# Kernel tuning notes

Hardware: AMD Instinct MI355X
Metric: run time of the kernel (lower is better)

The kernel has to match this reference:

```python
import jax, jax.numpy as jnp
import numpy as np

N_AA = 21
A = 15
D_FEAT = 128
D_COORD = N_AA * A * 3            # 945
D_DIH = 3 * (3 * 2 * 2 + 1)       # 39
D_IN = D_FEAT + D_COORD + D_DIH + D_FEAT  # 1240
FREQ = np.array([1.0, 2.0, 3.0, 1.0, 0.5, 1.0 / 3.0], dtype=np.float32)


def setup_inputs() -> dict:
    key = jax.random.key(0)
    ks = jax.random.split(key, 16)
    B, L = 16, 2048
    seq_idx = jax.random.randint(ks[0], (B, L), 0, N_AA)
    xyz = jax.random.normal(ks[1], (B, L, A, 3), dtype=jnp.float32)
    orientation = jax.random.normal(ks[2], (B, L, 3, 3), dtype=jnp.float32)
    dihedrals = jax.random.normal(ks[3], (B, L, 3), dtype=jnp.float32)
    chain_idx = jax.random.randint(ks[4], (B, L), 0, 10)
    atom_mask = jnp.ones((B, L, A), dtype=jnp.float32)
    aa_emb = jax.random.normal(ks[5], (N_AA, D_FEAT), dtype=jnp.float32) * 0.02
    chain_emb = jax.random.normal(ks[6], (10, D_FEAT), dtype=jnp.float32) * 0.02
    chain_emb = chain_emb.at[0].set(0.0)  # padding_idx=0
    W1 = jax.random.normal(ks[7], (D_IN, 2 * D_FEAT), dtype=jnp.float32) * 0.02
    b1 = jnp.zeros((2 * D_FEAT,), dtype=jnp.float32)
    W2 = jax.random.normal(ks[8], (2 * D_FEAT, D_FEAT), dtype=jnp.float32) * 0.02
    b2 = jnp.zeros((D_FEAT,), dtype=jnp.float32)
    W3 = jax.random.normal(ks[9], (D_FEAT, D_FEAT), dtype=jnp.float32) * 0.02
    b3 = jnp.zeros((D_FEAT,), dtype=jnp.float32)
    W4 = jax.random.normal(ks[10], (D_FEAT, D_FEAT), dtype=jnp.float32) * 0.02
    b4 = jnp.zeros((D_FEAT,), dtype=jnp.float32)
    return {"seq_idx": seq_idx, "xyz": xyz, "orientation": orientation,
            "dihedrals": dihedrals, "chain_idx": chain_idx, "atom_mask": atom_mask,
            "aa_emb": aa_emb, "chain_emb": chain_emb,
            "W1": W1, "b1": b1, "W2": W2, "b2": b2,
            "W3": W3, "b3": b3, "W4": W4, "b4": b4}


def _forward(seq_idx, xyz, orientation, dihedrals, chain_idx, atom_mask,
             aa_emb, chain_emb, W1, b1, W2, b2, W3, b3, W4, b4):
    B, L = seq_idx.shape
    CA = 1
    aa_type_feat = aa_emb[seq_idx]                                  # [B,L,F]
    xyz_rel = xyz - xyz[:, :, CA:CA + 1, :]                         # [B,L,A,3]
    # xyz_local[...,a,i] = sum_j R[b,l,j,i] * xyz_rel[b,l,a,j] (R^T applied)
    xyz_local = jnp.einsum('blji,blaj->blai', orientation, xyz_rel)
    xyz_local = xyz_local * atom_mask[..., None]
    # one-hot scatter into the residue-type slot (equiv to expanded where-select)
    onehot = jax.nn.one_hot(seq_idx, N_AA, dtype=xyz.dtype)         # [B,L,T]
    coord_feat = jnp.einsum('blt,blad->bltad', onehot, xyz_local)
    coord_feat = coord_feat.reshape(B, L, D_COORD)
    # angular encoding of dihedrals
    x = dihedrals[..., None]                                        # [B,L,3,1]
    freq = jnp.asarray(FREQ, dtype=dihedrals.dtype)
    enc = jnp.concatenate([x, jnp.sin(freq * x), jnp.cos(freq * x)], axis=-1)
    dihedral_feat = enc.reshape(B, L, D_DIH)
    chain_feat = chain_emb[chain_idx]                               # [B,L,F]
    feats = jnp.concatenate([aa_type_feat, coord_feat, dihedral_feat, chain_feat], axis=-1)
    h = jax.nn.relu(feats @ W1 + b1)
    h = jax.nn.relu(h @ W2 + b2)
    h = jax.nn.relu(h @ W3 + b3)
    return h @ W4 + b4


def reference(seq_idx, xyz, orientation, dihedrals, chain_idx, atom_mask,
              aa_emb, chain_emb, W1, b1, W2, b2, W3, b3, W4, b4):
    return _forward(seq_idx, xyz, orientation, dihedrals, chain_idx, atom_mask,
                    aa_emb, chain_emb, W1, b1, W2, b2, W3, b3, W4, b4)
```

## Files before the change

### kernel.cpp

```cpp
#include <hip/hip_runtime.h>
#include <math.h>

#define N_AA 21
#define NATOM 15
#define DF 128
#define H1DIM 256
#define OFF_COORD 128
#define OFF_DIH 1073
#define OFF_CHAIN 1112
#define T 16
#define FT 32
#define DIH0 46
#define HS1 264
#define HS2 136
#define FS 104
#define NFRAG_CH 16
#define INVALID_IDX 0xFFFFFFFFu
#define SSTRIDE 260

#define PR_TAB 31
#define PR_WF 16
#define PR_WL 63

typedef __attribute__((ext_vector_type(8))) short s16x8;
typedef __attribute__((ext_vector_type(4))) float f32x4;

__constant__ float c_freq[6] = {1.0f, 2.0f, 3.0f, 1.0f, 0.5f, 1.0f / 3.0f};

#define FMA4(A, S, W)            \
  A.x = fmaf((S), (W).x, A.x);   \
  A.y = fmaf((S), (W).y, A.y);   \
  A.z = fmaf((S), (W).z, A.z);   \
  A.w = fmaf((S), (W).w, A.w);

__device__ inline float bf2f(unsigned short u) {
  union { unsigned int i; float f; } x;
  x.i = (unsigned)u << 16;
  return x.f;
}
__device__ inline unsigned short f2bf(float f) {
  unsigned int x = __float_as_uint(f);
  unsigned int r = (x + 0x7fffu + ((x >> 16) & 1u)) >> 16;
  return (unsigned short)r;
}

__global__ __launch_bounds__(256) void prep_all(
    const float* __restrict__ aa_emb, const float* __restrict__ chain_emb,
    const float* __restrict__ W1, const float* __restrict__ b1,
    const float* __restrict__ W2, const float* __restrict__ W3,
    const float* __restrict__ W4, const int* __restrict__ seq, int n,
    float* __restrict__ tabAA, float* __restrict__ tabCH,
    unsigned short* __restrict__ wf_hi, unsigned short* __restrict__ wf_lo,
    unsigned short* __restrict__ wl1, int* __restrict__ part) {
  __shared__ float s_stage[32 * SSTRIDE];
  __shared__ int s_h[N_AA];
  const int b = blockIdx.x;
  if (b < PR_TAB) {
    const int i = threadIdx.x;
    if (b < N_AA) {
      const float* e = aa_emb + b * DF;
      float acc = 0.f;
#pragma unroll 8
      for (int k = 0; k < DF; ++k) acc = fmaf(e[k], W1[k * H1DIM + i], acc);
      tabAA[b * H1DIM + i] = acc;
    } else {
      const int c = b - N_AA;
      const float* e = chain_emb + c * DF;
      float acc = b1[i];
#pragma unroll 8
      for (int k = 0; k < DF; ++k)
        acc = fmaf(e[k], W1[(OFF_CHAIN + k) * H1DIM + i], acc);
      tabCH[c * H1DIM + i] = acc;
    }
  } else if (b < PR_TAB + PR_WF) {
    const int cgb = b - PR_TAB;
    const float* W;
    int kbase;
    if (cgb < 8) { W = W2; kbase = cgb * 32; }
    else if (cgb < 12) { W = W3; kbase = (cgb - 8) * 32; }
    else { W = W4; kbase = (cgb - 12) * 32; }
    for (int idx = threadIdx.x; idx < 32 * 128; idx += 256) {
      const int k = idx >> 7, col = idx & 127;
      s_stage[k * SSTRIDE + col] = W[(kbase + k) * DF + col];
    }
    __syncthreads();
    for (int e = threadIdx.x; e < 8 * 512; e += 256) {
      const int rem = e & 511;
      const int nt = e >> 9;
      const int l = rem >> 3, jj = rem & 7;
      const int col = nt * 16 + (l & 15);
      const int k = (l >> 4) * 8 + jj;
      const float v = s_stage[k * SSTRIDE + col];
      const unsigned short h = f2bf(v);
      wf_hi[(size_t)cgb * 4096 + e] = h;
      wf_lo[(size_t)cgb * 4096 + e] = f2bf(v - bf2f(h));
    }
  } else if (b < PR_TAB + PR_WF + PR_WL) {
    const int b2 = b - PR_TAB - PR_WF;
    const int t = b2 / 3, c = b2 % 3;
    for (int idx = threadIdx.x; idx < 32 * 256; idx += 256) {
      const int kp = idx >> 8, col = idx & 255;
      const int k = c * 32 + kp;
      float v = 0.f;
      if (k < 45) v = W1[(OFF_COORD + t * 45 + k) * H1DIM + col];
      else if (k < 84) v = W1[(OFF_DIH + (k - 45)) * H1DIM + col];
      s_stage[kp * SSTRIDE + col] = v;
    }
    __syncthreads();
    for (int e = threadIdx.x; e < 16 * 512; e += 256) {
      const int rem = e & 511;
      const int nt = e >> 9;
      const int l = rem >> 3, j = rem & 7;
      const int col = nt * 16 + (l & 15);
      const int kp = (l >> 4) * 8 + j;
      wl1[(size_t)b2 * 8192 + e] = f2bf(s_stage[kp * SSTRIDE + col]);
    }
  } else {
    const int hb = b - PR_TAB - PR_WF - PR_WL;
    if (threadIdx.x < N_AA) s_h[threadIdx.x] = 0;
    __syncthreads();
    const int i = hb * 256 + threadIdx.x;
    if (i < n) atomicAdd(&s_h[seq[i]], 1);
    __syncthreads();
    if (threadIdx.x < N_AA) part[hb * N_AA + threadIdx.x] = s_h[threadIdx.x];
  }
}

__global__ __launch_bounds__(256) void scatter_pad(
    const int* __restrict__ seq, int n, int cap, int nblkH,
    const int* __restrict__ part, int* __restrict__ totals,
    unsigned int* __restrict__ perm) {
  __shared__ int ps_tot[N_AA][9];
  __shared__ int ps_base[N_AA][9];
  __shared__ int s_tot[N_AA];
  __shared__ int s_base[N_AA];
  __shared__ int s_off[N_AA + 1];
  __shared__ int h[N_AA];
  const int b = blockIdx.x;
  const int myhb = b - N_AA - 1;
  const int tid = threadIdx.x;
  const int segLen = (nblkH + 7) >> 3;
  if (tid < N_AA * 8) {
    const int t = tid >> 3, seg = tid & 7;
    int tot = 0, bas = 0;
    for (int j = 0; j < segLen; ++j) {
      const int hb = seg * segLen + j;
      if (hb < nblkH) {
        const int v = part[hb * N_AA + t];
        tot += v;
        if (hb < myhb) bas += v;
      }
    }
    ps_tot[t][seg] = tot;
    ps_base[t][seg] = bas;
  }
  __syncthreads();
  if (tid < N_AA) {
    int tot = 0, bas = 0;
#pragma unroll
    for (int s = 0; s < 8; ++s) { tot += ps_tot[tid][s]; bas += ps_base[tid][s]; }
    s_tot[tid] = tot;
    s_base[tid] = bas;
  }
  __syncthreads();
  if (tid == 0) {
    int acc = 0;
    s_off[0] = 0;
    for (int tt = 0; tt < N_AA; ++tt) {
      acc += (s_tot[tt] + 15) & ~15;
      s_off[tt + 1] = acc;
    }
  }
  __syncthreads();
  if (b < N_AA) {
    const int padstart = s_off[b] + s_tot[b];
    const int padcnt = s_off[b + 1] - padstart;
    if (tid < padcnt) perm[padstart + tid] = INVALID_IDX;
  } else if (b == N_AA) {
    for (int i = s_off[N_AA] + tid; i < cap; i += 256) perm[i] = INVALID_IDX;
    if (tid < N_AA) totals[tid] = s_tot[tid];
  } else {
    if (tid < N_AA) h[tid] = 0;
    __syncthreads();
    const int i = myhb * 256 + tid;
    if (i < n) {
      const int tt = seq[i];
      const int slot = atomicAdd(&h[tt], 1);
      perm[s_off[tt] + s_base[tt] + slot] = (unsigned int)i;
    }
  }
}

__global__ __launch_bounds__(256, 8) void residue_embed_sorted(
    const float* __restrict__ xyz, const float* __restrict__ orient,
    const float* __restrict__ dihedrals, const int* __restrict__ chain_idx,
    const float* __restrict__ amask, const float* __restrict__ b2,
    const float* __restrict__ b3, const float* __restrict__ b4,
    const float* __restrict__ tabAA, const float* __restrict__ tabCH,
    const unsigned short* __restrict__ wl1, const unsigned short* __restrict__ wf_hi,
    const unsigned short* __restrict__ wf_lo, const int* __restrict__ totals,
    const unsigned int* __restrict__ perm, float* __restrict__ out) {
  __shared__ unsigned short s_h1hi[T][HS1];
  __shared__ __align__(16) char s_u[T * HS2 * 2];
  __shared__ unsigned int s_g[T];
  __shared__ int s_c[T];
  __shared__ int s_off[N_AA + 1];
  __shared__ int s_cnt[N_AA];

  unsigned short (*s_fh)[FS] = (unsigned short(*)[FS])s_u;
  unsigned short (*s_h2hi)[HS2] = (unsigned short(*)[HS2])s_u;

  const int tid = threadIdx.x;
  const int base = blockIdx.x * T;

  if (tid < T) {
    const unsigned int g = perm[base + tid];
    s_g[tid] = g;
    s_c[tid] = (g != INVALID_IDX) ? chain_idx[g] : 0;
  }
  if (tid >= 32 && tid < 32 + N_AA) s_cnt[tid - 32] = totals[tid - 32];
  __syncthreads();
  if (tid == 0) {
    int acc = 0;
    s_off[0] = 0;
    for (int t2 = 0; t2 < N_AA; ++t2) {
      acc += (s_cnt[t2] + 15) & ~15;
      s_off[t2 + 1] = acc;
    }
  }

  for (int idx = tid; idx < T * 45; idx += 256) {
    const int r = idx / 45, k = idx % 45;
    const int a = k / 3, i = k % 3;
    const unsigned int g = s_g[r];
    float v = 0.f;
    if (g != INVALID_IDX) {
      const float* X = xyz + (size_t)g * 45;
      const float* R = orient + (size_t)g * 9;
      const float m = amask[(size_t)g * NATOM + a];
#pragma unroll
      for (int j = 0; j < 3; ++j)
        v = fmaf(R[j * 3 + i], X[a * 3 + j] - X[3 + j], v);
      v *= m;
    }
    s_fh[r][k] = f2bf(v);
  }
  for (int idx = tid; idx < T * 39; idx += 256) {
    const int r = idx / 39, kk = idx % 39;
    const int d = kk / 13, m = kk % 13;
    const unsigned int g = s_g[r];
    float v = 0.f;
    if (g != INVALID_IDX) {
      const float x = dihedrals[(size_t)g * 3 + d];
      if (m == 0) v = x;
      else if (m <= 6) v = sinf(c_freq[m - 1] * x);
      else v = cosf(c_freq[m - 7] * x);
    }
    s_fh[r][45 + kk] = f2bf(v);
  }
  for (int idx = tid; idx < T * 12; idx += 256) {
    const int r = idx / 12, k = 84 + idx % 12;
    s_fh[r][k] = 0;
  }
  __syncthreads();

  const int l = tid & 63;
  const int nc = tid >> 6;
  const int nc0 = nc * 32;
  const int ar = l & 15;
  const int kb = (l >> 4) * 8;
  const int drow = (l >> 4) * 4;
  const size_t fbase = (size_t)(2 * nc) * 512 + (size_t)l * 8;

  int ty = 0;
#pragma unroll
  for (int t2 = 1; t2 < N_AA; ++t2)
    if (base >= s_off[t2]) ty = t2;

  {
    f32x4 acc[4] = {{0.f, 0.f, 0.f, 0.f}, {0.f, 0.f, 0.f, 0.f},
                    {0.f, 0.f, 0.f, 0.f}, {0.f, 0.f, 0.f, 0.f}};
    s16x8 ah[3];
#pragma unroll
    for (int c = 0; c < 3; ++c)
      ah[c] = *(const s16x8*)(&s_fh[ar][c * 32 + kb]);
    const unsigned short* pB = wl1 + ((size_t)ty * 48 + 4 * nc) * 512 + (size_t)l * 8;
#pragma unroll
    for (int c = 0; c < 3; ++c) {
#pragma unroll
      for (int nt2 = 0; nt2 < 4; ++nt2) {
        const s16x8 bb = *(const s16x8*)(pB + ((size_t)c * 16 + nt2) * 512);
        acc[nt2] = __builtin_amdgcn_mfma_f32_16x16x32_bf16(ah[c], bb, acc[nt2], 0, 0, 0);
      }
    }
    __syncthreads();
#pragma unroll
    for (int nt2 = 0; nt2 < 4; ++nt2) {
      const int col0 = nc * 64 + nt2 * 16 + (l & 15);
      const float ta = tabAA[ty * H1DIM + col0];
#pragma unroll
      for (int reg = 0; reg < 4; ++reg) {
        const int row = drow + reg;
        float v = acc[nt2][reg] + ta + tabCH[s_c[row] * H1DIM + col0];
        v = fmaxf(v, 0.f);
        s_h1hi[row][col0] = f2bf(v);
      }
    }
  }
  __syncthreads();

#define MFMA_LAYER(NCHUNK, CG0, SRCH, SSTR, BPTR, EPI)                           \
  do {                                                                           \
    f32x4 acc0 = {0.f, 0.f, 0.f, 0.f}, acc1 = {0.f, 0.f, 0.f, 0.f};             \
    const unsigned short* ph = wf_hi + (size_t)(CG0)*4096 + fbase;               \
    const unsigned short* pl = wf_lo + (size_t)(CG0)*4096 + fbase;               \
    _Pragma("unroll 2")                                                          \
    for (int c = 0; c < (NCHUNK); ++c) {                                         \
      const s16x8 b0h = *(const s16x8*)(ph + (size_t)c * 4096);                  \
      const s16x8 b1h = *(const s16x8*)(ph + (size_t)c * 4096 + 512);            \
      const s16x8 b0l = *(const s16x8*)(pl + (size_t)c * 4096);                  \
      const s16x8 b1l = *(const s16x8*)(pl + (size_t)c * 4096 + 512);            \
      const int ko = c * 32 + kb;                                                \
      const s16x8 ah = *(const s16x8*)((SRCH) + ar * (SSTR) + ko);               \
      acc0 = __builtin_amdgcn_mfma_f32_16x16x32_bf16(ah, b0h, acc0, 0, 0, 0);    \
      acc1 = __builtin_amdgcn_mfma_f32_16x16x32_bf16(ah, b1h, acc1, 0, 0, 0);    \
      acc0 = __builtin_amdgcn_mfma_f32_16x16x32_bf16(ah, b0l, acc0, 0, 0, 0);    \
      acc1 = __builtin_amdgcn_mfma_f32_16x16x32_bf16(ah, b1l, acc1, 0, 0, 0);    \
    }                                                                            \
    const float bias0 = (BPTR)[nc0 + (l & 15)];                                  \
    const float bias1 = (BPTR)[nc0 + 16 + (l & 15)];                             \
    EPI                                                                          \
  } while (0)

#define EPI_HIDDEN(DH, DSTR)                                                     \
  {                                                                              \
    _Pragma("unroll")                                                            \
    for (int reg = 0; reg < 4; ++reg) {                                          \
      const int row = drow + reg;                                                \
      float v0 = fmaxf(acc0[reg] + bias0, 0.f);                                  \
      float v1 = fmaxf(acc1[reg] + bias1, 0.f);                                  \
      (DH)[row * (DSTR) + nc0 + (l & 15)] = f2bf(v0);                            \
      (DH)[row * (DSTR) + nc0 + 16 + (l & 15)] = f2bf(v1);                       \
    }                                                                            \
  }

  MFMA_LAYER(8, 0, &s_h1hi[0][0], HS1, b2, EPI_HIDDEN(&s_h2hi[0][0], HS2));
  __syncthreads();

  MFMA_LAYER(4, 8, &s_h2hi[0][0], HS2, b3, EPI_HIDDEN(&s_h1hi[0][0], HS1));
  __syncthreads();

  MFMA_LAYER(4, 12, &s_h1hi[0][0], HS1, b4, {
    _Pragma("unroll")
    for (int reg = 0; reg < 4; ++reg) {
      const unsigned int g = s_g[drow + reg];
      if (g != INVALID_IDX) {
        out[(size_t)g * DF + nc0 + (l & 15)] = acc0[reg] + bias0;
        out[(size_t)g * DF + nc0 + 16 + (l & 15)] = acc1[reg] + bias1;
      }
    }
  });
}

__global__ __launch_bounds__(256) void precompute_tables(
    const float* __restrict__ aa_emb, const float* __restrict__ chain_emb,
    const float* __restrict__ W1, const float* __restrict__ b1,
    float* __restrict__ tabAA, float* __restrict__ tabCH) {
  const int i = threadIdx.x;
  const int b = blockIdx.x;
  if (b < N_AA) {
    const float* e = aa_emb + b * DF;
    float acc = 0.f;
#pragma unroll 8
    for (int k = 0; k < DF; ++k) acc = fmaf(e[k], W1[k * H1DIM + i], acc);
    tabAA[b * H1DIM + i] = acc;
  } else {
    const int c = b - N_AA;
    const float* e = chain_emb + c * DF;
    float acc = b1[i];
#pragma unroll 8
    for (int k = 0; k < DF; ++k)
      acc = fmaf(e[k], W1[(OFF_CHAIN + k) * H1DIM + i], acc);
    tabCH[c * H1DIM + i] = acc;
  }
}

__global__ __launch_bounds__(512, 4) void residue_embed_fallback(
    const int* __restrict__ seq_idx, const float* __restrict__ xyz,
    const float* __restrict__ orient, const float* __restrict__ dihedrals,
    const int* __restrict__ chain_idx, const float* __restrict__ amask,
    const float* __restrict__ W1, const float* __restrict__ W2,
    const float* __restrict__ b2, const float* __restrict__ W3,
    const float* __restrict__ b3, const float* __restrict__ W4,
    const float* __restrict__ b4, const float* __restrict__ tabAA,
    const float* __restrict__ tabCH, float* __restrict__ out) {
  __shared__ float s_h1[FT][260];
  __shared__ float s_buf2[FT][132];
  __shared__ float s_w[32 * DF];
  __shared__ int s_t[FT];
  __shared__ int s_c[FT];

  const int tid = threadIdx.x;
  const int base = blockIdx.x * FT;

  if (tid < FT) {
    s_t[tid] = seq_idx[base + tid];
    s_c[tid] = chain_idx[base + tid];
  }
  for (int idx = tid; idx < FT * 45; idx += 512) {
    const int r = idx / 45, k = idx % 45;
    const int a = k / 3, i = k % 3;
    const int g = base + r;
    const float* X = xyz + g * 45;
    const float* R = orient + g * 9;
    const float m = amask[g * NATOM + a];
    float v = 0.f;
#pragma unroll
    for (int j = 0; j < 3; ++j)
      v = fmaf(R[j * 3 + i], X[a * 3 + j] - X[3 + j], v);
    s_buf2[r][k] = v * m;
  }
  for (int idx = tid; idx < FT * 39; idx += 512) {
    const int r = idx / 39, k = idx % 39;
    const int d = k / 13, m = k % 13;
    const float x = dihedrals[(base + r) * 3 + d];
    float v;
    if (m == 0) v = x;
    else if (m <= 6) v = sinf(c_freq[m - 1] * x);
    else v = cosf(c_freq[m - 7] * x);
    s_buf2[r][DIH0 + k] = v;
  }
  __syncthreads();
  {
    const int i0 = (tid & 63) * 4;
    const int r0 = (tid >> 6) * 4;
    float4 acc[4];
#pragma unroll
    for (int rr = 0; rr < 4; ++rr) {
      const int t = s_t[r0 + rr], c = s_c[r0 + rr];
      const float4 a = *(const float4*)(tabAA + t * H1DIM + i0);
      const float4 b = *(const float4*)(tabCH + c * H1DIM + i0);
      acc[rr].x = a.x + b.x; acc[rr].y = a.y + b.y;
      acc[rr].z = a.z + b.z; acc[rr].w = a.w + b.w;
    }
#pragma unroll 3
    for (int k = 0; k < 39; ++k) {
      const float4 wv = *(const float4*)(W1 + (OFF_DIH + k) * H1DIM + i0);
#pragma unroll
      for (int rr = 0; rr < 4; ++rr) {
        FMA4(acc[rr], s_buf2[r0 + rr][DIH0 + k], wv);
      }
    }
    const float* wp[4];
#pragma unroll
    for (int rr = 0; rr < 4; ++rr)
      wp[rr] = W1 + (OFF_COORD + s_t[r0 + rr] * 45) * H1DIM + i0;
    for (int k = 0; k < 45; ++k) {
#pragma unroll
      for (int rr = 0; rr < 4; ++rr) {
        const float4 wv = *(const float4*)(wp[rr] + k * H1DIM);
        FMA4(acc[rr], s_buf2[r0 + rr][k], wv);
      }
    }
#pragma unroll
    for (int rr = 0; rr < 4; ++rr) {
      float4 v;
      v.x = fmaxf(acc[rr].x, 0.f); v.y = fmaxf(acc[rr].y, 0.f);
      v.z = fmaxf(acc[rr].z, 0.f); v.w = fmaxf(acc[rr].w, 0.f);
      *(float4*)(&s_h1[r0 + rr][i0]) = v;
    }
  }
  const int j0 = (tid & 31) * 4;
  const int r2 = (tid >> 5) * 2;
#define FB_LAYER(NCH, WSRC, SRC, BPTR, STORE)                               \
  do {                                                                      \
    const float4 bb = *(const float4*)((BPTR) + j0);                        \
    float4 acc0 = bb, acc1 = bb;                                            \
    for (int c = 0; c < (NCH); ++c) {                                       \
      __syncthreads();                                                      \
      {                                                                     \
        const float* src = (WSRC) + c * 32 * DF;                            \
        const int idx = tid * 8;                                            \
        *(float4*)(&s_w[idx]) = *(const float4*)(src + idx);                \
        *(float4*)(&s_w[idx + 4]) = *(const float4*)(src + idx + 4);        \
      }                                                                     \
      __syncthreads();                                                      \
      const int kb2 = c * 32;                                               \
      _Pragma("unroll")                                                     \
      for (int kk = 0; kk < 32; kk += 4) {                                  \
        const float4 a0 = *(const float4*)(&(SRC)[r2][kb2 + kk]);           \
        const float4 a1 = *(const float4*)(&(SRC)[r2 + 1][kb2 + kk]);       \
        const float4 w0 = *(const float4*)(&s_w[(kk + 0) * DF + j0]);       \
        const float4 w1 = *(const float4*)(&s_w[(kk + 1) * DF + j0]);       \
        const float4 w2 = *(const float4*)(&s_w[(kk + 2) * DF + j0]);       \
        const float4 w3 = *(const float4*)(&s_w[(kk + 3) * DF + j0]);       \
        FMA4(acc0, a0.x, w0); FMA4(acc1, a1.x, w0);                         \
        FMA4(acc0, a0.y, w1); FMA4(acc1, a1.y, w1);                         \
        FMA4(acc0, a0.z, w2); FMA4(acc1, a1.z, w2);                         \
        FMA4(acc0, a0.w, w3); FMA4(acc1, a1.w, w3);                         \
      }                                                                     \
    }                                                                       \
    STORE                                                                   \
  } while (0)
#define RELU_STORE(DST)                                                     \
  {                                                                         \
    float4 v0, v1;                                                          \
    v0.x = fmaxf(acc0.x, 0.f); v0.y = fmaxf(acc0.y, 0.f);                   \
    v0.z = fmaxf(acc0.z, 0.f); v0.w = fmaxf(acc0.w, 0.f);                   \
    v1.x = fmaxf(acc1.x, 0.f); v1.y = fmaxf(acc1.y, 0.f);                   \
    v1.z = fmaxf(acc1.z, 0.f); v1.w = fmaxf(acc1.w, 0.f);                   \
    *(float4*)(&(DST)[r2][j0]) = v0;                                        \
    *(float4*)(&(DST)[r2 + 1][j0]) = v1;                                    \
  }
  FB_LAYER(8, W2, s_h1, b2, RELU_STORE(s_buf2));
  FB_LAYER(4, W3, s_buf2, b3, RELU_STORE(s_h1));
  FB_LAYER(4, W4, s_h1, b4, {
    *(float4*)(out + (size_t)(base + r2) * DF + j0) = acc0;
    *(float4*)(out + (size_t)(base + r2 + 1) * DF + j0) = acc1;
  });
}

extern "C" void kernel_launch(void* const* d_in, const int* in_sizes, int n_in,
                              void* d_out, int out_size, void* d_ws, size_t ws_size,
                              hipStream_t stream) {
  const int* seq = (const int*)d_in[0];
  const float* xyz = (const float*)d_in[1];
  const float* orient = (const float*)d_in[2];
  const float* dihedrals = (const float*)d_in[3];
  const int* chain = (const int*)d_in[4];
  const float* amask = (const float*)d_in[5];
  const float* aa_emb = (const float*)d_in[6];
  const float* chain_emb = (const float*)d_in[7];
  const float* W1 = (const float*)d_in[8];
  const float* b1 = (const float*)d_in[9];
  const float* W2 = (const float*)d_in[10];
  const float* b2 = (const float*)d_in[11];
  const float* W3 = (const float*)d_in[12];
  const float* b3 = (const float*)d_in[13];
  const float* W4 = (const float*)d_in[14];
  const float* b4 = (const float*)d_in[15];
  float* out = (float*)d_out;
  const int n_res = in_sizes[0];

  const int nblkH = (n_res + 255) / 256;

  char* wsp = (char*)d_ws;
  const size_t o_tabAA = 0;
  const size_t o_tabCH = o_tabAA + (size_t)N_AA * H1DIM * 4;
  const size_t o_wfhi = (o_tabCH + (size_t)10 * H1DIM * 4 + 255) & ~255ull;
  const size_t o_wflo = o_wfhi + (size_t)NFRAG_CH * 8 * 512 * 2;
  const size_t o_wl1 = o_wflo + (size_t)NFRAG_CH * 8 * 512 * 2;
  const size_t wl1_bytes = (size_t)N_AA * 3 * 16 * 512 * 2;
  const size_t o_part = (o_wl1 + wl1_bytes + 255) & ~255ull;
  const size_t o_tot = (o_part + (size_t)nblkH * N_AA * 4 + 255) & ~255ull;
  const size_t o_perm = (o_tot + N_AA * 4 + 255) & ~255ull;
  const int npad_max = n_res + N_AA * 15;
  const int nblkB = (npad_max + T - 1) / T;
  const int cap = nblkB * T;
  const size_t perm_bytes = (size_t)cap * 4;
  const size_t need = o_perm + perm_bytes;

  float* tabAA = (float*)(wsp + o_tabAA);
  float* tabCH = (float*)(wsp + o_tabCH);

  if (ws_size >= need) {
    unsigned short* wf_hi = (unsigned short*)(wsp + o_wfhi);
    unsigned short* wf_lo = (unsigned short*)(wsp + o_wflo);
    unsigned short* wl1 = (unsigned short*)(wsp + o_wl1);
    int* part = (int*)(wsp + o_part);
    int* totals = (int*)(wsp + o_tot);
    unsigned int* perm = (unsigned int*)(wsp + o_perm);

    const int nprep = PR_TAB + PR_WF + PR_WL + nblkH;
    hipLaunchKernelGGL(prep_all, dim3(nprep), dim3(256), 0, stream, aa_emb,
                       chain_emb, W1, b1, W2, W3, W4, seq, n_res, tabAA, tabCH,
                       wf_hi, wf_lo, wl1, part);

    hipLaunchKernelGGL(scatter_pad, dim3(nblkH + N_AA + 1), dim3(256), 0,
                       stream, seq, n_res, cap, nblkH, part, totals, perm);

    hipLaunchKernelGGL(residue_embed_sorted, dim3(nblkB), dim3(256), 0, stream,
                       xyz, orient, dihedrals, chain, amask, b2, b3, b4, tabAA,
                       tabCH, wl1, wf_hi, wf_lo, totals, perm, out);
  } else {
    hipLaunchKernelGGL(precompute_tables, dim3(N_AA + 10), dim3(256), 0, stream,
                       aa_emb, chain_emb, W1, b1, tabAA, tabCH);
    const int nblk = n_res / FT;
    hipLaunchKernelGGL(residue_embed_fallback, dim3(nblk), dim3(512), 0, stream,
                       seq, xyz, orient, dihedrals, chain, amask, W1, W2, b2,
                       W3, b3, W4, b4, tabAA, tabCH, out);
  }
}
```

Before: 59.49 us.

## Fuse prep and scatter into cooperative kernel; prefetch MLP weight fragments across barriers

Merges the prep and scatter_pad launches into one cooperative kernel that separates the two phases with a grid-wide sync, and falls back to two launches if the cooperative launch fails. This removes one kernel launch and its inter-kernel gap. In the main kernel, the first weight fragments of each MLP layer are loaded before the preceding barrier so the load latency overlaps the sync, and some redundant __syncthreads are removed. The grid sync adds its own cost and depends on every block being co-resident. Removing barriers risks races on the shared buffers.

```diff
diff --git a/kernel.cpp b/kernel.cpp
--- a/kernel.cpp
+++ b/kernel.cpp
@@ -1,4 +1,5 @@
 #include <hip/hip_runtime.h>
+#include <hip/hip_cooperative_groups.h>
 #include <math.h>
 
 #define N_AA 21
@@ -44,7 +45,8 @@
   return (unsigned short)r;
 }
 
-__global__ __launch_bounds__(256) void prep_all(
+__device__ inline void prep_role(
+    int b, int tid, float* s_stage, int* s_h,
     const float* __restrict__ aa_emb, const float* __restrict__ chain_emb,
     const float* __restrict__ W1, const float* __restrict__ b1,
     const float* __restrict__ W2, const float* __restrict__ W3,
@@ -52,11 +54,8 @@
     float* __restrict__ tabAA, float* __restrict__ tabCH,
     unsigned short* __restrict__ wf_hi, unsigned short* __restrict__ wf_lo,
     unsigned short* __restrict__ wl1, int* __restrict__ part) {
-  __shared__ float s_stage[32 * SSTRIDE];
-  __shared__ int s_h[N_AA];
-  const int b = blockIdx.x;
   if (b < PR_TAB) {
-    const int i = threadIdx.x;
+    const int i = tid;
     if (b < N_AA) {
       const float* e = aa_emb + b * DF;
       float acc = 0.f;
@@ -79,12 +78,12 @@
     if (cgb < 8) { W = W2; kbase = cgb * 32; }
     else if (cgb < 12) { W = W3; kbase = (cgb - 8) * 32; }
     else { W = W4; kbase = (cgb - 12) * 32; }
-    for (int idx = threadIdx.x; idx < 32 * 128; idx += 256) {
+    for (int idx = tid; idx < 32 * 128; idx += 256) {
       const int k = idx >> 7, col = idx & 127;
       s_stage[k * SSTRIDE + col] = W[(kbase + k) * DF + col];
     }
     __syncthreads();
-    for (int e = threadIdx.x; e < 8 * 512; e += 256) {
+    for (int e = tid; e < 8 * 512; e += 256) {
       const int rem = e & 511;
       const int nt = e >> 9;
       const int l = rem >> 3, jj = rem & 7;
@@ -98,7 +97,7 @@
   } else if (b < PR_TAB + PR_WF + PR_WL) {
     const int b2 = b - PR_TAB - PR_WF;
     const int t = b2 / 3, c = b2 % 3;
-    for (int idx = threadIdx.x; idx < 32 * 256; idx += 256) {
+    for (int idx = tid; idx < 32 * 256; idx += 256) {
       const int kp = idx >> 8, col = idx & 255;
       const int k = c * 32 + kp;
       float v = 0.f;
@@ -107,7 +106,7 @@
       s_stage[kp * SSTRIDE + col] = v;
     }
     __syncthreads();
-    for (int e = threadIdx.x; e < 16 * 512; e += 256) {
+    for (int e = tid; e < 16 * 512; e += 256) {
       const int rem = e & 511;
       const int nt = e >> 9;
       const int l = rem >> 3, j = rem & 7;
@@ -117,28 +116,21 @@
     }
   } else {
     const int hb = b - PR_TAB - PR_WF - PR_WL;
-    if (threadIdx.x < N_AA) s_h[threadIdx.x] = 0;
+    if (tid < N_AA) s_h[tid] = 0;
     __syncthreads();
-    const int i = hb * 256 + threadIdx.x;
+    const int i = hb * 256 + tid;
     if (i < n) atomicAdd(&s_h[seq[i]], 1);
     __syncthreads();
-    if (threadIdx.x < N_AA) part[hb * N_AA + threadIdx.x] = s_h[threadIdx.x];
-  }
-}
-
-__global__ __launch_bounds__(256) void scatter_pad(
-    const int* __restrict__ seq, int n, int cap, int nblkH,
-    const int* __restrict__ part, int* __restrict__ totals,
+    if (tid < N_AA) part[hb * N_AA + tid] = s_h[tid];
+  }
+}
+
+__device__ inline void scatter_role(
+    int b, int tid, int (*ps_tot)[9], int (*ps_base)[9], int* s_tot,
+    int* s_base, int* s_off, int* h, const int* __restrict__ seq, int n,
+    int cap, int nblkH, const int* __restrict__ part, int* __restrict__ totals,
     unsigned int* __restrict__ perm) {
-  __shared__ int ps_tot[N_AA][9];
-  __shared__ int ps_base[N_AA][9];
-  __shared__ int s_tot[N_AA];
-  __shared__ int s_base[N_AA];
-  __shared__ int s_off[N_AA + 1];
-  __shared__ int h[N_AA];
-  const int b = blockIdx.x;
   const int myhb = b - N_AA - 1;
-  const int tid = threadIdx.x;
   const int segLen = (nblkH + 7) >> 3;
   if (tid < N_AA * 8) {
     const int t = tid >> 3, seg = tid & 7;
@@ -191,6 +183,57 @@
   }
 }
 
+__global__ __launch_bounds__(256) void prep_scatter(
+    const float* aa_emb, const float* chain_emb, const float* W1,
+    const float* b1, const float* W2, const float* W3, const float* W4,
+    const int* seq, int n, float* tabAA, float* tabCH,
+    unsigned short* wf_hi, unsigned short* wf_lo, unsigned short* wl1,
+    int* part, int cap, int nblkH, int* totals, unsigned int* perm) {
+  __shared__ float s_stage[32 * SSTRIDE];
+  __shared__ int s_h[N_AA];
+  __shared__ int ps_tot[N_AA][9];
+  __shared__ int ps_base[N_AA][9];
+  __shared__ int s_tot[N_AA];
+  __shared__ int s_base[N_AA];
+  __shared__ int s_off[N_AA + 1];
+  const int b = blockIdx.x;
+  const int tid = threadIdx.x;
+  prep_role(b, tid, s_stage, s_h, aa_emb, chain_emb, W1, b1, W2, W3, W4, seq,
+            n, tabAA, tabCH, wf_hi, wf_lo, wl1, part);
+  cooperative_groups::this_grid().sync();
+  if (b < nblkH + N_AA + 1)
+    scatter_role(b, tid, ps_tot, ps_base, s_tot, s_base, s_off, s_h, seq, n,
+                 cap, nblkH, part, totals, perm);
+}
+
+__global__ __launch_bounds__(256) void prep_all(
+    const float* __restrict__ aa_emb, const float* __restrict__ chain_emb,
+    const float* __restrict__ W1, const float* __restrict__ b1,
+    const float* __restrict__ W2, const float* __restrict__ W3,
+    const float* __restrict__ W4, const int* __restrict__ seq, int n,
+    float* __restrict__ tabAA, float* __restrict__ tabCH,
+    unsigned short* __restrict__ wf_hi, unsigned short* __restrict__ wf_lo,
+    unsigned short* __restrict__ wl1, int* __restrict__ part) {
+  __shared__ float s_stage[32 * SSTRIDE];
+  __shared__ int s_h[N_AA];
+  prep_role(blockIdx.x, threadIdx.x, s_stage, s_h, aa_emb, chain_emb, W1, b1,
+            W2, W3, W4, seq, n, tabAA, tabCH, wf_hi, wf_lo, wl1, part);
+}
+
+__global__ __launch_bounds__(256) void scatter_pad(
+    const int* __restrict__ seq, int n, int cap, int nblkH,
+    const int* __restrict__ part, int* __restrict__ totals,
+    unsigned int* __restrict__ perm) {
+  __shared__ int ps_tot[N_AA][9];
+  __shared__ int ps_base[N_AA][9];
+  __shared__ int s_tot[N_AA];
+  __shared__ int s_base[N_AA];
+  __shared__ int s_off[N_AA + 1];
+  __shared__ int h[N_AA];
+  scatter_role(blockIdx.x, threadIdx.x, ps_tot, ps_base, s_tot, s_base, s_off,
+               h, seq, n, cap, nblkH, part, totals, perm);
+}
+
 __global__ __launch_bounds__(256, 8) void residue_embed_sorted(
     const float* __restrict__ xyz, const float* __restrict__ orient,
     const float* __restrict__ dihedrals, const int* __restrict__ chain_idx,
@@ -293,7 +336,6 @@
         acc[nt2] = __builtin_amdgcn_mfma_f32_16x16x32_bf16(ah[c], bb, acc[nt2], 0, 0, 0);
       }
     }
-    __syncthreads();
 #pragma unroll
     for (int nt2 = 0; nt2 < 4; ++nt2) {
       const int col0 = nc * 64 + nt2 * 16 + (l & 15);
@@ -307,15 +349,32 @@
       }
     }
   }
-  __syncthreads();
-
-#define MFMA_LAYER(NCHUNK, CG0, SRCH, SSTR, BPTR, EPI)                           \
+
+#define PRELOAD_FRAGS(P, CG0)                                                    \
+  s16x8 P##b0h, P##b1h, P##b0l, P##b1l;                                          \
+  {                                                                              \
+    const unsigned short* ph_ = wf_hi + (size_t)(CG0)*4096 + fbase;              \
+    const unsigned short* pl_ = wf_lo + (size_t)(CG0)*4096 + fbase;              \
+    P##b0h = *(const s16x8*)(ph_);                                               \
+    P##b1h = *(const s16x8*)(ph_ + 512);                                         \
+    P##b0l = *(const s16x8*)(pl_);                                               \
+    P##b1l = *(const s16x8*)(pl_ + 512);                                         \
+  }
+
+#define MFMA_LAYER_P(NCHUNK, CG0, P, SRCH, SSTR, BPTR, EPI)                      \
   do {                                                                           \
     f32x4 acc0 = {0.f, 0.f, 0.f, 0.f}, acc1 = {0.f, 0.f, 0.f, 0.f};             \
     const unsigned short* ph = wf_hi + (size_t)(CG0)*4096 + fbase;               \
     const unsigned short* pl = wf_lo + (size_t)(CG0)*4096 + fbase;               \
+    {                                                                            \
+      const s16x8 ah = *(const s16x8*)((SRCH) + ar * (SSTR) + kb);               \
+      acc0 = __builtin_amdgcn_mfma_f32_16x16x32_bf16(ah, P##b0h, acc0, 0, 0, 0); \
+      acc1 = __builtin_amdgcn_mfma_f32_16x16x32_bf16(ah, P##b1h, acc1, 0, 0, 0); \
+      acc0 = __builtin_amdgcn_mfma_f32_16x16x32_bf16(ah, P##b0l, acc0, 0, 0, 0); \
+      acc1 = __builtin_amdgcn_mfma_f32_16x16x32_bf16(ah, P##b1l, acc1, 0, 0, 0); \
+    }                                                                            \
     _Pragma("unroll 2")                                                          \
-    for (int c = 0; c < (NCHUNK); ++c) {                                         \
+    for (int c = 1; c < (NCHUNK); ++c) {                                         \
       const s16x8 b0h = *(const s16x8*)(ph + (size_t)c * 4096);                  \
       const s16x8 b1h = *(const s16x8*)(ph + (size_t)c * 4096 + 512);            \
       const s16x8 b0l = *(const s16x8*)(pl + (size_t)c * 4096);                  \
@@ -344,13 +403,18 @@
     }                                                                            \
   }
 
-  MFMA_LAYER(8, 0, &s_h1hi[0][0], HS1, b2, EPI_HIDDEN(&s_h2hi[0][0], HS2));
-  __syncthreads();
-
-  MFMA_LAYER(4, 8, &s_h2hi[0][0], HS2, b3, EPI_HIDDEN(&s_h1hi[0][0], HS1));
-  __syncthreads();
-
-  MFMA_LAYER(4, 12, &s_h1hi[0][0], HS1, b4, {
+  PRELOAD_FRAGS(p2, 0);
+  __syncthreads();
+
+  MFMA_LAYER_P(8, 0, p2, &s_h1hi[0][0], HS1, b2, EPI_HIDDEN(&s_h2hi[0][0], HS2));
+  PRELOAD_FRAGS(p3, 8);
+  __syncthreads();
+
+  MFMA_LAYER_P(4, 8, p3, &s_h2hi[0][0], HS2, b3, EPI_HIDDEN(&s_h1hi[0][0], HS1));
+  PRELOAD_FRAGS(p4, 12);
+  __syncthreads();
+
+  MFMA_LAYER_P(4, 12, p4, &s_h1hi[0][0], HS1, b4, {
     _Pragma("unroll")
     for (int reg = 0; reg < 4; ++reg) {
       const unsigned int g = s_g[drow + reg];
@@ -572,12 +636,25 @@
     unsigned int* perm = (unsigned int*)(wsp + o_perm);
 
     const int nprep = PR_TAB + PR_WF + PR_WL + nblkH;
-    hipLaunchKernelGGL(prep_all, dim3(nprep), dim3(256), 0, stream, aa_emb,
-                       chain_emb, W1, b1, W2, W3, W4, seq, n_res, tabAA, tabCH,
-                       wf_hi, wf_lo, wl1, part);
-
-    hipLaunchKernelGGL(scatter_pad, dim3(nblkH + N_AA + 1), dim3(256), 0,
-                       stream, seq, n_res, cap, nblkH, part, totals, perm);
+
+    int n_arg = n_res, cap_arg = cap, nblkH_arg = nblkH;
+    void* cargs[] = {(void*)&aa_emb, (void*)&chain_emb, (void*)&W1, (void*)&b1,
+                     (void*)&W2, (void*)&W3, (void*)&W4, (void*)&seq,
+                     (void*)&n_arg, (void*)&tabAA, (void*)&tabCH,
+                     (void*)&wf_hi, (void*)&wf_lo, (void*)&wl1, (void*)&part,
+                     (void*)&cap_arg, (void*)&nblkH_arg, (void*)&totals,
+                     (void*)&perm};
+    hipError_t cerr = hipLaunchCooperativeKernel(
+        (const void*)prep_scatter, dim3(nprep), dim3(256), (void**)cargs, 0,
+        stream);
+    if (cerr != hipSuccess) {
+      (void)hipGetLastError();
+      hipLaunchKernelGGL(prep_all, dim3(nprep), dim3(256), 0, stream, aa_emb,
+                         chain_emb, W1, b1, W2, W3, W4, seq, n_res, tabAA,
+                         tabCH, wf_hi, wf_lo, wl1, part);
+      hipLaunchKernelGGL(scatter_pad, dim3(nblkH + N_AA + 1), dim3(256), 0,
+                         stream, seq, n_res, cap, nblkH, part, totals, perm);
+    }
 
     hipLaunchKernelGGL(residue_embed_sorted, dim3(nblkB), dim3(256), 0, stream,
                        xyz, orient, dihedrals, chain, amask, b2, b3, b4, tabAA,
```

Result: slower. 95.39 us (+60.3%).
